# Optimization experiments

Hardware: AMD Instinct MI355X
Metric: run time of the kernel (lower is better)

Reference implementation:

```python
import jax, jax.numpy as jnp
import numpy as np

NUM_HEADS = 3
WIN = 7            # window_size (square)
PAD = WIN // 2     # conv / v padding


def setup_inputs() -> dict:
    key = jax.random.key(0)
    ks = jax.random.split(key, 8)
    B, C, H, W = 8, 96, 56, 56
    hd = C // NUM_HEADS  # 32
    x = jax.random.normal(ks[0], (B, C, H, W), jnp.float32)
    # qkv 1x1 conv: weight (3C, C), bias (3C,)
    w_qkv = jax.random.normal(ks[1], (3 * C, C), jnp.float32) * (C ** -0.5)
    b_qkv = jax.random.normal(ks[2], (3 * C,), jnp.float32) * 0.01
    fan_in = 2 * hd * WIN * WIN
    w_dm = jax.random.normal(ks[3], (WIN * WIN, 2 * hd, WIN, WIN), jnp.float32) * (fan_in ** -0.5)
    b_dm = jax.random.normal(ks[4], (WIN * WIN,), jnp.float32) * 0.01
    bias_table = jax.random.normal(ks[5], (WIN * WIN, NUM_HEADS), jnp.float32) * 0.02
    # proj 1x1 conv
    w_proj = jax.random.normal(ks[6], (C, C), jnp.float32) * (C ** -0.5)
    b_proj = jax.random.normal(ks[7], (C,), jnp.float32) * 0.01
    return dict(x=x, w_qkv=w_qkv, b_qkv=b_qkv, w_dm=w_dm, b_dm=b_dm,
                bias_table=bias_table, w_proj=w_proj, b_proj=b_proj)


def reference(x, w_qkv, b_qkv, w_dm, b_dm, bias_table, w_proj, b_proj):
    B, C, H, W = x.shape
    nh = NUM_HEADS
    hd = C // nh
    scale = hd ** -0.5

    # qkv 1x1 conv -> (B, 3, nh, hd, H, W)
    qkv = jnp.einsum('oc,bchw->bohw', w_qkv, x) + b_qkv[None, :, None, None]
    qkv = qkv.reshape(B, 3, nh, hd, H, W)
    q, k, v = qkv[:, 0], qkv[:, 1], qkv[:, 2]

    qk = jnp.concatenate([(q * scale).reshape(B * nh, hd, H, W),
                          k.reshape(B * nh, hd, H, W)], axis=1)
    attn = jax.lax.conv_general_dilated(
        qk, w_dm, window_strides=(1, 1), padding=[(PAD, PAD), (PAD, PAD)],
        dimension_numbers=('NCHW', 'OIHW', 'NCHW')) + b_dm[None, :, None, None]
    attn = attn.reshape(B, nh, WIN * WIN, H, W)

    # relative position bias, broadcast over spatial dims
    attn = attn + bias_table.T.reshape(1, nh, WIN * WIN, 1, 1)
    attn = jax.nn.softmax(attn, axis=2)

    # gather sliding windows of v from a zero-padded tensor
    v_pad = jnp.pad(v, ((0, 0), (0, 0), (0, 0), (PAD, PAD), (PAD, PAD)))
    vw = jnp.stack([v_pad[..., i // WIN:i // WIN + H, i % WIN:i % WIN + W]
                    for i in range(WIN * WIN)], axis=3)

    # weighted sum over window dim, merge heads back to channels
    out = jnp.sum(vw * attn[:, :, None], axis=3).reshape(B, C, H, W)

    # output 1x1 projection (dropout p=0 -> identity)
    out = jnp.einsum('oc,bchw->bohw', w_proj, out) + b_proj[None, :, None, None]
    return out
```

## Files before the change

kernel.cpp:

```cpp
#include <hip/hip_runtime.h>
#include <hip/hip_bf16.h>
#include <stdint.h>

#define BATCH 8
#define CCH 96
#define NH 3
#define HD 32
#define HGT 56
#define WID 56
#define HW 3136
#define WIN 7
#define KK 49
#define PADR 3
#define NIMG 24
#define C2 64

typedef const float* fp32p;
typedef __attribute__((ext_vector_type(8))) short bf16x8;
typedef __attribute__((ext_vector_type(16))) float f32x16;
typedef unsigned short ushort_t;

__device__ __forceinline__ float bf2f_bits(unsigned u){ return __uint_as_float(u << 16); }
__device__ __forceinline__ ushort_t f2bf_bits(float f){
  __hip_bfloat16 hb = __float2bfloat16(f);
  return *(ushort_t*)&hb;
}

__global__ void prep_kernel(fp32p w_dm, fp32p b_dm, fp32p bias_table,
                            fp32p w_qkv, fp32p w_proj,
                            __hip_bfloat16* __restrict__ w3, float* __restrict__ bias3,
                            ushort_t* __restrict__ wq3, ushort_t* __restrict__ wp3){
  int t = blockIdx.x * 256 + threadIdx.x;
  if (t < 200704){
    int j   = t & 7;
    int l   = (t >> 3) & 63;
    int mt  = (t >> 9) & 1;
    int cb  = (t >> 10) & 1;
    int pt  = t >> 11;
    int pass = pt / KK, tap = pt % KK;
    int o  = mt*32 + (l & 31);
    int ch = pass*32 + cb*16 + (l >> 5)*8 + j;
    float v = 0.f;
    if (o < KK) v = w_dm[((size_t)(o*C2 + ch))*KK + tap];
    w3[t] = __float2bfloat16(v);
  } else if (t < 200896){
    int t2 = t - 200704;
    int h = t2 >> 6;
    int o = t2 & 63;
    bias3[t2] = (o < KK) ? (b_dm[o] + bias_table[o*NH + h]) : -1e30f;
  } else if (t < 200896 + 27648){
    int i = t - 200896;
    int j = i & 7, l = (i >> 3) & 63;
    int rest = i >> 9;
    int mt = rest % 9, k = rest / 9;
    int o = mt*32 + (l & 31);
    int c = k*16 + (l >> 5)*8 + j;
    wq3[i] = f2bf_bits(w_qkv[o*CCH + c]);
  } else if (t < 200896 + 27648 + 9216){
    int i = t - 200896 - 27648;
    int j = i & 7, l = (i >> 3) & 63;
    int rest = i >> 9;
    int mt = rest % 3, k = rest / 3;
    int o = mt*32 + (l & 31);
    int c = k*16 + (l >> 5)*8 + j;
    wp3[i] = f2bf_bits(w_proj[o*CCH + c]);
  }
}

__global__ __launch_bounds__(256) void xt_kernel(fp32p x, ushort_t* __restrict__ xbf){
  __shared__ float lds[128*97];
  int px0 = blockIdx.x * 128;
  int tid = threadIdx.x;
  #pragma unroll
  for (int it = 0; it < 48; ++it){
    int s = tid + it*256;
    int px = s & 127;
    int c  = s >> 7;
    int gpx = px0 + px;
    int b = gpx / HW, pp = gpx % HW;
    lds[px*97 + c] = x[((size_t)b*CCH + c)*HW + pp];
  }
  __syncthreads();
  #pragma unroll
  for (int it = 0; it < 6; ++it){
    int s = tid + it*256;
    int j  = s % 12;
    int px = s / 12;
    unsigned u[4];
    #pragma unroll
    for (int q = 0; q < 4; ++q){
      float f0 = lds[px*97 + j*8 + 2*q];
      float f1 = lds[px*97 + j*8 + 2*q + 1];
      u[q] = (unsigned)f2bf_bits(f0) | ((unsigned)f2bf_bits(f1) << 16);
    }
    uint4 w4; w4.x=u[0]; w4.y=u[1]; w4.z=u[2]; w4.w=u[3];
    *(uint4*)((char*)xbf + ((size_t)(px0+px)*96 + j*8)*2) = w4;
  }
}

__global__ __launch_bounds__(64) void qkv_kernel(const ushort_t* __restrict__ xbf,
    const ushort_t* __restrict__ wq3, fp32p b_qkv,
    ushort_t* __restrict__ qplane, ushort_t* __restrict__ kplane,
    ushort_t* __restrict__ v2){
  int wid = blockIdx.x;
  int g  = wid / 784;
  int pt = wid % 784;
  int l = threadIdx.x & 63, col = l & 31, hi = l >> 5;
  int px = pt*32 + col;
  int b = px / HW, pp = px % HW;

  bf16x8 B[6];
  const char* bb = (const char*)xbf + (size_t)px*192 + hi*16;
  #pragma unroll
  for (int k = 0; k < 6; ++k) B[k] = *(const bf16x8*)(bb + k*32);

  f32x16 acc[3];
  #pragma unroll
  for (int m = 0; m < 3; ++m)
    #pragma unroll
    for (int r = 0; r < 16; ++r) acc[m][r] = 0.f;

  #pragma unroll
  for (int k = 0; k < 6; ++k){
    #pragma unroll
    for (int m = 0; m < 3; ++m){
      bf16x8 A = *(const bf16x8*)((const char*)wq3 + ((size_t)((k*9 + g*3 + m)*64 + l))*16);
      acc[m] = __builtin_amdgcn_mfma_f32_32x32x16_bf16(A, B[k], acc[m], 0, 0, 0);
    }
  }
  const float scale = 0.17677669529663687f;
  ushort_t* plane = (g == 0) ? qplane : (g == 1 ? kplane : v2);
  #pragma unroll
  for (int m = 0; m < 3; ++m){
    ushort_t* dst = plane + ((size_t)((b*NH + m)*HW + pp))*32;
    #pragma unroll
    for (int q = 0; q < 4; ++q){
      int base = 8*q + 4*hi;
      float v0 = acc[m][q*4+0] + b_qkv[g*96 + m*32 + base + 0];
      float v1 = acc[m][q*4+1] + b_qkv[g*96 + m*32 + base + 1];
      float v2f = acc[m][q*4+2] + b_qkv[g*96 + m*32 + base + 2];
      float v3 = acc[m][q*4+3] + b_qkv[g*96 + m*32 + base + 3];
      if (g == 0){ v0 *= scale; v1 *= scale; v2f *= scale; v3 *= scale; }
      uint2 pk;
      pk.x = (unsigned)f2bf_bits(v0) | ((unsigned)f2bf_bits(v1) << 16);
      pk.y = (unsigned)f2bf_bits(v2f) | ((unsigned)f2bf_bits(v3) << 16);
      *(uint2*)(&dst[base]) = pk;
    }
  }
}

#define MFMA4(Ab, Bb) \
  { _Pragma("unroll") for (int cb = 0; cb < 2; ++cb){ \
      acc[0] = __builtin_amdgcn_mfma_f32_32x32x16_bf16(Ab[cb][0], Bb[cb], acc[0], 0, 0, 0); \
      acc[1] = __builtin_amdgcn_mfma_f32_32x32x16_bf16(Ab[cb][1], Bb[cb], acc[1], 0, 0, 0); \
    } }

#define LOADA(tt, Ab) \
  { const char* An_ = Abase + (size_t)(tt)*4096; \
    _Pragma("unroll") for (int cb = 0; cb < 2; ++cb) \
      _Pragma("unroll") for (int mt = 0; mt < 2; ++mt) \
        Ab[cb][mt] = *(const bf16x8*)(An_ + (cb*2 + mt)*1024); }

#define LOADB(tt, Bb) \
  { int ky_ = (tt) / 7, kx_ = (tt) - ky_*7; \
    int xp_ = nth*32 + col + kx_; if (xp_ > 61) xp_ = 61; \
    int base_ = ((row + ky_)*64 + xp_)*64; \
    int sx_ = (xp_ & 3) ^ ((xp_ >> 2) & 3); \
    _Pragma("unroll") for (int cb = 0; cb < 2; ++cb) \
      Bb[cb] = *(const bf16x8*)(&smem[base_ + ((((cb << 1) | hi) ^ sx_) << 4)]); }

__global__ __launch_bounds__(256, 3) void attn_kernel(
    const ushort_t* __restrict__ qplane, const ushort_t* __restrict__ kplane,
    const __hip_bfloat16* __restrict__ w3, const float* __restrict__ bias3,
    const ushort_t* __restrict__ v2, ushort_t* __restrict__ tmp2){
  __shared__ char smem[50176];

  int bid = blockIdx.x;
  int n  = bid / 28;
  int y0 = (bid % 28) * 2;
  int b = n / NH, head = n % NH;
  int tid = threadIdx.x;
  int l = tid & 63, w = tid >> 6, hi = l >> 5, col = l & 31;
  int row = w >> 1;
  int nth = w & 1;

  f32x16 acc[2];
  #pragma unroll
  for (int r = 0; r < 16; ++r){
    int rowv = (r & 3) + 8*(r >> 2) + 4*hi;
    acc[0][r] = bias3[head*64 + rowv];
    acc[1][r] = bias3[head*64 + 32 + rowv];
  }

  for (int pass = 0; pass < 2; ++pass){
    if (pass) __syncthreads();
    const char* src = (const char*)(pass ? kplane : qplane) + (size_t)n * HW * 64;
    #pragma unroll
    for (int it = 0; it < 8; ++it){
      int s = tid + it*256;
      int c   = s & 3;
      int xp  = (s >> 2) & 63;
      int rw  = s >> 8;
      int gy = y0 - 3 + rw;
      int gx = xp - 3;
      uint4 val = {0,0,0,0};
      if ((unsigned)gy < HGT && (unsigned)gx < WID)
        val = *(const uint4*)(src + (size_t)(gy*WID + gx)*64 + c*16);
      int sw = (c ^ (xp & 3) ^ ((xp >> 2) & 3)) << 4;
      *(uint4*)(&smem[(rw*64 + xp)*64 + sw]) = val;
    }
    __syncthreads();

    const char* Abase = (const char*)w3 + (size_t)pass*KK*4096 + l*16;
    bf16x8 A0[2][2], A1[2][2], B0[2], B1[2];
    LOADA(0, A0); LOADB(0, B0);
    LOADA(1, A1); LOADB(1, B1);
    for (int t = 0; t < 48; t += 2){
      MFMA4(A0, B0);
      LOADA(t+2, A0); LOADB(t+2, B0);
      MFMA4(A1, B1);
      int t3 = (t+3 < KK) ? (t+3) : 48;
      LOADA(t3, A1); LOADB(t3, B1);
    }
    MFMA4(A0, B0);
  }

  const char* vb = (const char*)v2 + (size_t)n * HW * 64;
  uint4 vreg[8];
  #pragma unroll
  for (int it = 0; it < 8; ++it){
    int s = tid + it*256;
    int xp  = s & 63;
    int c   = (s >> 6) & 3;
    int rw  = s >> 8;
    int gy = y0 - 3 + rw;
    int gx = xp - 3;
    uint4 val = {0,0,0,0};
    if ((unsigned)gy < HGT && (unsigned)gx < WID)
      val = *(const uint4*)(vb + (size_t)(gy*WID + gx)*64 + c*16);
    vreg[it] = val;
  }

  ushort_t* Pp = (ushort_t*)&smem[32768];
  {
    float m = -1e30f;
    #pragma unroll
    for (int r = 0; r < 16; ++r){ m = fmaxf(m, acc[0][r]); m = fmaxf(m, acc[1][r]); }
    m = fmaxf(m, __shfl_xor(m, 32));
    float s = 0.f;
    #pragma unroll
    for (int r = 0; r < 16; ++r){
      acc[0][r] = __expf(acc[0][r] - m); s += acc[0][r];
      acc[1][r] = __expf(acc[1][r] - m); s += acc[1][r];
    }
    s += __shfl_xor(s, 32);
    float inv = 1.f / s;
    int pixslot = row*64 + nth*32 + col;
    ushort_t* Pr = Pp + pixslot*68;
    #pragma unroll
    for (int q = 0; q < 4; ++q){
      int base = 8*q + 4*hi;
      uint2 pk0;
      pk0.x = (unsigned)f2bf_bits(acc[0][q*4+0]*inv) | ((unsigned)f2bf_bits(acc[0][q*4+1]*inv) << 16);
      pk0.y = (unsigned)f2bf_bits(acc[0][q*4+2]*inv) | ((unsigned)f2bf_bits(acc[0][q*4+3]*inv) << 16);
      *(uint2*)(&Pr[base]) = pk0;
      uint2 pk1;
      pk1.x = (unsigned)f2bf_bits(acc[1][q*4+0]*inv) | ((unsigned)f2bf_bits(acc[1][q*4+1]*inv) << 16);
      pk1.y = (unsigned)f2bf_bits(acc[1][q*4+2]*inv) | ((unsigned)f2bf_bits(acc[1][q*4+3]*inv) << 16);
      *(uint2*)(&Pr[32 + base]) = pk1;
    }
  }
  __syncthreads();

  #pragma unroll
  for (int it = 0; it < 8; ++it){
    int s = tid + it*256;
    int xp  = s & 63;
    int c   = (s >> 6) & 3;
    int rw  = s >> 8;
    *(uint4*)(&smem[((c*8 + rw)*64 + xp)*16]) = vreg[it];
  }
  __syncthreads();

  int ch2 = tid >> 7;
  int slot = tid & 127;
  int pr = slot >> 6, pxx = slot & 63;
  if (pxx < WID){
    float out[16];
    #pragma unroll
    for (int i = 0; i < 16; ++i) out[i] = 0.f;
    #pragma unroll
    for (int ky = 0; ky < WIN; ++ky){
      #pragma unroll
      for (int kx = 0; kx < WIN; ++kx){
        float pw = bf2f_bits(Pp[slot*68 + ky*7 + kx]);
        int vrow = pr + ky, xp = pxx + kx;
        #pragma unroll
        for (int ci = 0; ci < 2; ++ci){
          int cc = ch2*2 + ci;
          uint4 vv = *(const uint4*)(&smem[((cc*8 + vrow)*64 + xp)*16]);
          unsigned ua[4] = {vv.x, vv.y, vv.z, vv.w};
          #pragma unroll
          for (int q = 0; q < 4; ++q){
            out[ci*8 + 2*q]     = fmaf(pw, __uint_as_float(ua[q] << 16),         out[ci*8 + 2*q]);
            out[ci*8 + 2*q + 1] = fmaf(pw, __uint_as_float(ua[q] & 0xffff0000u), out[ci*8 + 2*q + 1]);
          }
        }
      }
    }
    int pp = (y0 + pr)*WID + pxx;
    ushort_t* dst = tmp2 + ((size_t)(b*HW + pp))*96 + head*32 + ch2*16;
    #pragma unroll
    for (int j2 = 0; j2 < 2; ++j2){
      unsigned u[4];
      #pragma unroll
      for (int q = 0; q < 4; ++q){
        u[q] = (unsigned)f2bf_bits(out[j2*8 + 2*q]) | ((unsigned)f2bf_bits(out[j2*8 + 2*q + 1]) << 16);
      }
      uint4 w4; w4.x=u[0]; w4.y=u[1]; w4.z=u[2]; w4.w=u[3];
      *(uint4*)(&dst[j2*8]) = w4;
    }
  }
}

__global__ __launch_bounds__(64) void proj_kernel(const ushort_t* __restrict__ tmp2,
    const ushort_t* __restrict__ wp3, fp32p b_proj, float* __restrict__ outp){
  int pt = blockIdx.x;
  int l = threadIdx.x & 63, col = l & 31, hi = l >> 5;
  int px = pt*32 + col;
  int b = px / HW, pp = px % HW;

  bf16x8 B[6];
  const char* bb = (const char*)tmp2 + (size_t)px*192 + hi*16;
  #pragma unroll
  for (int k = 0; k < 6; ++k) B[k] = *(const bf16x8*)(bb + k*32);

  f32x16 acc[3];
  #pragma unroll
  for (int m = 0; m < 3; ++m)
    #pragma unroll
    for (int r = 0; r < 16; ++r) acc[m][r] = 0.f;

  #pragma unroll
  for (int k = 0; k < 6; ++k){
    #pragma unroll
    for (int m = 0; m < 3; ++m){
      bf16x8 A = *(const bf16x8*)((const char*)wp3 + ((size_t)((k*3 + m)*64 + l))*16);
      acc[m] = __builtin_amdgcn_mfma_f32_32x32x16_bf16(A, B[k], acc[m], 0, 0, 0);
    }
  }
  #pragma unroll
  for (int m = 0; m < 3; ++m){
    #pragma unroll
    for (int r = 0; r < 16; ++r){
      int o = m*32 + (r & 3) + 8*(r >> 2) + 4*hi;
      outp[((size_t)(b*CCH + o))*HW + pp] = acc[m][r] + b_proj[o];
    }
  }
}

extern "C" void kernel_launch(void* const* d_in, const int* in_sizes, int n_in,
                              void* d_out, int out_size, void* d_ws, size_t ws_size,
                              hipStream_t stream){
  fp32p x          = (fp32p)d_in[0];
  fp32p w_qkv      = (fp32p)d_in[1];
  fp32p b_qkv      = (fp32p)d_in[2];
  fp32p w_dm       = (fp32p)d_in[3];
  fp32p b_dm       = (fp32p)d_in[4];
  fp32p bias_table = (fp32p)d_in[5];
  fp32p w_proj     = (fp32p)d_in[6];
  fp32p b_proj     = (fp32p)d_in[7];

  char* ws = (char*)d_ws;
  const size_t XBF_BYTES   = (size_t)BATCH * HW * 96 * 2;
  const size_t PLANE_BYTES = (size_t)NIMG * HW * 32 * 2;
  const size_t TMP2_BYTES  = (size_t)BATCH * HW * 96 * 2;
  const size_t W3_BYTES    = 200704ull * 2;
  size_t off = 0;
  ushort_t* xbf    = (ushort_t*)(ws + off); off += XBF_BYTES;
  ushort_t* qplane = (ushort_t*)(ws + off); off += PLANE_BYTES;
  ushort_t* kplane = (ushort_t*)(ws + off); off += PLANE_BYTES;
  ushort_t* v2     = (ushort_t*)(ws + off); off += PLANE_BYTES;
  ushort_t* tmp2   = (ushort_t*)(ws + off); off += TMP2_BYTES;
  __hip_bfloat16* w3 = (__hip_bfloat16*)(ws + off); off += W3_BYTES;
  float* bias3     = (float*)(ws + off);    off += 192*4;
  ushort_t* wq3    = (ushort_t*)(ws + off); off += 27648*2;
  ushort_t* wp3    = (ushort_t*)(ws + off); off += 9216*2;

  hipLaunchKernelGGL(prep_kernel, dim3(929), dim3(256), 0, stream,
                     w_dm, b_dm, bias_table, w_qkv, w_proj, w3, bias3, wq3, wp3);
  hipLaunchKernelGGL(xt_kernel, dim3(196), dim3(256), 0, stream, x, xbf);
  hipLaunchKernelGGL(qkv_kernel, dim3(2352), dim3(64), 0, stream,
                     xbf, wq3, b_qkv, qplane, kplane, v2);
  hipLaunchKernelGGL(attn_kernel, dim3(672), dim3(256), 0, stream,
                     qplane, kplane, w3, bias3, v2, tmp2);
  hipLaunchKernelGGL(proj_kernel, dim3(784), dim3(64), 0, stream,
                     tmp2, wp3, b_proj, (float*)d_out);
}
```

Measured before the change: 84.18 us.

## Split attention-score MFMA reduction across waves by channel block (split-K)

The per-wave work split in the score convolution changes from splitting output pixels (two 32-pixel halves) to splitting the reduction channels (two 16-channel blocks). Each wave now computes partial sums for all 64 pixels of its row, and the partials are exchanged through swizzled shared memory and summed before the softmax. The aim is to halve the A-operand (weight) loads per wave and change the load-to-MFMA balance. In exchange it doubles the accumulator registers, which risks occupancy under the 256x3 launch bound, and adds an extra LDS exchange with two barriers.

New measurement: 78.04 us. 7.3% less time.

```diff
diff --git a/kernel.cpp b/kernel.cpp
--- a/kernel.cpp
+++ b/kernel.cpp
@@ -149,25 +149,39 @@
   }
 }
 
-#define MFMA4(Ab, Bb) \
-  { _Pragma("unroll") for (int cb = 0; cb < 2; ++cb){ \
-      acc[0] = __builtin_amdgcn_mfma_f32_32x32x16_bf16(Ab[cb][0], Bb[cb], acc[0], 0, 0, 0); \
-      acc[1] = __builtin_amdgcn_mfma_f32_32x32x16_bf16(Ab[cb][1], Bb[cb], acc[1], 0, 0, 0); \
+#define MFMA4K(Ab, Bb) \
+  { _Pragma("unroll") for (int nt = 0; nt < 2; ++nt){ \
+      acc[0][nt] = __builtin_amdgcn_mfma_f32_32x32x16_bf16(Ab[0], Bb[nt], acc[0][nt], 0, 0, 0); \
+      acc[1][nt] = __builtin_amdgcn_mfma_f32_32x32x16_bf16(Ab[1], Bb[nt], acc[1][nt], 0, 0, 0); \
     } }
 
-#define LOADA(tt, Ab) \
+#define LOADAK(tt, Ab) \
   { const char* An_ = Abase + (size_t)(tt)*4096; \
-    _Pragma("unroll") for (int cb = 0; cb < 2; ++cb) \
-      _Pragma("unroll") for (int mt = 0; mt < 2; ++mt) \
-        Ab[cb][mt] = *(const bf16x8*)(An_ + (cb*2 + mt)*1024); }
-
-#define LOADB(tt, Bb) \
+    Ab[0] = *(const bf16x8*)(An_); \
+    Ab[1] = *(const bf16x8*)(An_ + 1024); }
+
+#define LOADBK(tt, Bb) \
   { int ky_ = (tt) / 7, kx_ = (tt) - ky_*7; \
-    int xp_ = nth*32 + col + kx_; if (xp_ > 61) xp_ = 61; \
-    int base_ = ((row + ky_)*64 + xp_)*64; \
-    int sx_ = (xp_ & 3) ^ ((xp_ >> 2) & 3); \
-    _Pragma("unroll") for (int cb = 0; cb < 2; ++cb) \
-      Bb[cb] = *(const bf16x8*)(&smem[base_ + ((((cb << 1) | hi) ^ sx_) << 4)]); }
+    _Pragma("unroll") for (int nt = 0; nt < 2; ++nt){ \
+      int xp_ = nt*32 + col + kx_; if (xp_ > 61) xp_ = 61; \
+      int base_ = ((row + ky_)*64 + xp_)*64; \
+      int sx_ = (xp_ & 3) ^ ((xp_ >> 2) & 3); \
+      Bb[nt] = *(const bf16x8*)(&smem[base_ + ((((cbw << 1) | hi) ^ sx_) << 4)]); } }
+
+#define XWRITE(A0v, A1v) \
+  { _Pragma("unroll") for (int q = 0; q < 4; ++q){ \
+      float4 v4; \
+      v4.x=A0v[4*q+0]; v4.y=A0v[4*q+1]; v4.z=A0v[4*q+2]; v4.w=A0v[4*q+3]; \
+      *(float4*)((char*)xch + slot_o*256 + (((2*q+hi) ^ xsw)<<4)) = v4; \
+      v4.x=A1v[4*q+0]; v4.y=A1v[4*q+1]; v4.z=A1v[4*q+2]; v4.w=A1v[4*q+3]; \
+      *(float4*)((char*)xch + slot_o*256 + (((8+2*q+hi) ^ xsw)<<4)) = v4; } }
+
+#define XREAD(A0v, A1v) \
+  { _Pragma("unroll") for (int q = 0; q < 4; ++q){ \
+      float4 v4 = *(const float4*)((char*)xch + slot_s*256 + (((2*q+hi) ^ xsw)<<4)); \
+      A0v[4*q+0]+=v4.x; A0v[4*q+1]+=v4.y; A0v[4*q+2]+=v4.z; A0v[4*q+3]+=v4.w; \
+      v4 = *(const float4*)((char*)xch + slot_s*256 + (((8+2*q+hi) ^ xsw)<<4)); \
+      A1v[4*q+0]+=v4.x; A1v[4*q+1]+=v4.y; A1v[4*q+2]+=v4.z; A1v[4*q+3]+=v4.w; } }
 
 __global__ __launch_bounds__(256, 3) void attn_kernel(
     const ushort_t* __restrict__ qplane, const ushort_t* __restrict__ kplane,
@@ -182,14 +196,16 @@
   int tid = threadIdx.x;
   int l = tid & 63, w = tid >> 6, hi = l >> 5, col = l & 31;
   int row = w >> 1;
-  int nth = w & 1;
-
-  f32x16 acc[2];
+  int cbw = w & 1;
+
+  f32x16 acc[2][2];
   #pragma unroll
   for (int r = 0; r < 16; ++r){
     int rowv = (r & 3) + 8*(r >> 2) + 4*hi;
-    acc[0][r] = bias3[head*64 + rowv];
-    acc[1][r] = bias3[head*64 + 32 + rowv];
+    float b0 = (cbw == 0) ? bias3[head*64 + rowv] : 0.f;
+    float b1 = (cbw == 0) ? bias3[head*64 + 32 + rowv] : 0.f;
+    #pragma unroll
+    for (int nt = 0; nt < 2; ++nt){ acc[0][nt][r] = b0; acc[1][nt][r] = b1; }
   }
 
   for (int pass = 0; pass < 2; ++pass){
@@ -211,18 +227,34 @@
     }
     __syncthreads();
 
-    const char* Abase = (const char*)w3 + (size_t)pass*KK*4096 + l*16;
-    bf16x8 A0[2][2], A1[2][2], B0[2], B1[2];
-    LOADA(0, A0); LOADB(0, B0);
-    LOADA(1, A1); LOADB(1, B1);
+    const char* Abase = (const char*)w3 + (size_t)pass*KK*4096 + cbw*2048 + l*16;
+    bf16x8 A0[2], A1[2], B0[2], B1[2];
+    LOADAK(0, A0); LOADBK(0, B0);
+    LOADAK(1, A1); LOADBK(1, B1);
     for (int t = 0; t < 48; t += 2){
-      MFMA4(A0, B0);
-      LOADA(t+2, A0); LOADB(t+2, B0);
-      MFMA4(A1, B1);
+      MFMA4K(A0, B0);
+      LOADAK(t+2, A0); LOADBK(t+2, B0);
+      MFMA4K(A1, B1);
       int t3 = (t+3 < KK) ? (t+3) : 48;
-      LOADA(t3, A1); LOADB(t3, B1);
-    }
-    MFMA4(A0, B0);
+      LOADAK(t3, A1); LOADBK(t3, B1);
+    }
+    MFMA4K(A0, B0);
+  }
+
+  __syncthreads();
+  float* xch = (float*)smem;
+  int xsw = col & 15;
+  {
+    int slot_o = row*64 + (1-cbw)*32 + col;
+    if (cbw == 0){ XWRITE(acc[0][1], acc[1][1]); }
+    else         { XWRITE(acc[0][0], acc[1][0]); }
+  }
+  __syncthreads();
+  f32x16 a0, a1;
+  {
+    int slot_s = row*64 + cbw*32 + col;
+    if (cbw == 0){ XREAD(acc[0][0], acc[1][0]); a0 = acc[0][0]; a1 = acc[1][0]; }
+    else         { XREAD(acc[0][1], acc[1][1]); a0 = acc[0][1]; a1 = acc[1][1]; }
   }
 
   const char* vb = (const char*)v2 + (size_t)n * HW * 64;
@@ -245,28 +277,28 @@
   {
     float m = -1e30f;
     #pragma unroll
-    for (int r = 0; r < 16; ++r){ m = fmaxf(m, acc[0][r]); m = fmaxf(m, acc[1][r]); }
+    for (int r = 0; r < 16; ++r){ m = fmaxf(m, a0[r]); m = fmaxf(m, a1[r]); }
     m = fmaxf(m, __shfl_xor(m, 32));
     float s = 0.f;
     #pragma unroll
     for (int r = 0; r < 16; ++r){
-      acc[0][r] = __expf(acc[0][r] - m); s += acc[0][r];
-      acc[1][r] = __expf(acc[1][r] - m); s += acc[1][r];
+      a0[r] = __expf(a0[r] - m); s += a0[r];
+      a1[r] = __expf(a1[r] - m); s += a1[r];
     }
     s += __shfl_xor(s, 32);
     float inv = 1.f / s;
-    int pixslot = row*64 + nth*32 + col;
+    int pixslot = row*64 + cbw*32 + col;
     ushort_t* Pr = Pp + pixslot*68;
     #pragma unroll
     for (int q = 0; q < 4; ++q){
       int base = 8*q + 4*hi;
       uint2 pk0;
-      pk0.x = (unsigned)f2bf_bits(acc[0][q*4+0]*inv) | ((unsigned)f2bf_bits(acc[0][q*4+1]*inv) << 16);
-      pk0.y = (unsigned)f2bf_bits(acc[0][q*4+2]*inv) | ((unsigned)f2bf_bits(acc[0][q*4+3]*inv) << 16);
+      pk0.x = (unsigned)f2bf_bits(a0[q*4+0]*inv) | ((unsigned)f2bf_bits(a0[q*4+1]*inv) << 16);
+      pk0.y = (unsigned)f2bf_bits(a0[q*4+2]*inv) | ((unsigned)f2bf_bits(a0[q*4+3]*inv) << 16);
       *(uint2*)(&Pr[base]) = pk0;
       uint2 pk1;
-      pk1.x = (unsigned)f2bf_bits(acc[1][q*4+0]*inv) | ((unsigned)f2bf_bits(acc[1][q*4+1]*inv) << 16);
-      pk1.y = (unsigned)f2bf_bits(acc[1][q*4+2]*inv) | ((unsigned)f2bf_bits(acc[1][q*4+3]*inv) << 16);
+      pk1.x = (unsigned)f2bf_bits(a1[q*4+0]*inv) | ((unsigned)f2bf_bits(a1[q*4+1]*inv) << 16);
+      pk1.y = (unsigned)f2bf_bits(a1[q*4+2]*inv) | ((unsigned)f2bf_bits(a1[q*4+3]*inv) << 16);
       *(uint2*)(&Pr[32 + base]) = pk1;
     }
   }
```
